# Performance work log

Measured on AMD Instinct MI355X. Metric: run time of the kernel, lower is better.

Reference implementation:

```python
import jax, jax.numpy as jnp
import numpy as np

N = 50000   # num_nodes
R = 16      # num_relations
B = 4       # num_bases = ceil(sqrt(R))
D = 128     # input_dim == output_dim -> vertical stacking path
E = 1_600_000  # num_edges = N * avg_degree(32)


def setup_inputs() -> dict:
    key = jax.random.key(0)
    ks = jax.random.split(key, 7)
    x = jax.random.normal(ks[0], (N, D), dtype=jnp.float32)
    source = jax.random.randint(ks[1], (E,), 0, N)
    target = jax.random.randint(ks[2], (E,), 0, N)
    edge_type = jax.random.randint(ks[3], (E,), 0, R)
    edge_weights = jax.random.uniform(ks[4], (E,), dtype=jnp.float32)
    # LowRankRepresentation params: weight (R, B) via uniform_norm_p1_ (uniform, L1-normalized),
    # bases (B, D, D) via xavier_normal_
    w = jax.random.uniform(ks[5], (R, B), dtype=jnp.float32)
    base_weights = w / jnp.sum(w, axis=-1, keepdims=True)
    xavier_std = (2.0 / (D + D)) ** 0.5
    bases = jax.random.normal(ks[6], (B, D, D), dtype=jnp.float32) * xavier_std
    return dict(x=x, source=source, target=target, edge_type=edge_type,
                edge_weights=edge_weights, base_weights=base_weights, bases=bases)


def reference(x, source, target, edge_type, edge_weights, base_weights, bases):
    # BasesDecomposition.forward, vertical stacking (input_dim == output_dim):
    #   adj: (R*N, N) sparse COO with indices (edge_type*N + target, source), values edge_weights
    #   h = spmm(adj, x)                -> (R*N, D), duplicate edges summed
    #   out = einsum('rb,bio,rni->no')  -> (N, D)
    num_nodes = x.shape[0]
    num_relations = base_weights.shape[0]
    seg = edge_type * num_nodes + target            # row index in stacked adjacency
    msgs = x[source] * edge_weights[:, None]        # (E, D) gathered + weighted messages
    h = jax.ops.segment_sum(msgs, seg, num_segments=num_relations * num_nodes)
    h = h.reshape(num_relations, num_nodes, -1)     # (R, N, D)
    return jnp.einsum('rb,bio,rni->no', base_weights, bases, h)
```

## Files before the change

### kernel.cpp

```cpp
#include <hip/hip_runtime.h>

#define NN 50000
#define NR 16
#define NB 4
#define DD 128
#define CAP 96

typedef __attribute__((ext_vector_type(8))) short bf16x8;
typedef __attribute__((ext_vector_type(4))) float f32x4;

static const size_t OFF_REC = (size_t)1 << 20;
static const size_t OFF_G   = (size_t)40 << 20;
static const size_t OFF_WF  = (size_t)96 << 20;

static __device__ __forceinline__ unsigned short f2bf(float f) {
    unsigned int u = __float_as_uint(f);
    unsigned int r = (u + 0x7FFF + ((u >> 16) & 1)) >> 16;
    return (unsigned short)r;
}

__global__ void fill_kernel(const int* __restrict__ src, const int* __restrict__ tgt,
                            const int* __restrict__ et, const float* __restrict__ ew,
                            int* __restrict__ cnt, int2* __restrict__ rec, int E) {
    int e = blockIdx.x * blockDim.x + threadIdx.x;
    if (e >= E) return;
    int t = tgt[e];
    int pos = atomicAdd(&cnt[t], 1);
    if (pos < CAP) {
        int2 r;
        r.x = src[e] | (et[e] << 16);
        r.y = __float_as_int(ew[e]);
        rec[t * CAP + pos] = r;
    }
}

__global__ void prep_kernel(const float* __restrict__ W, unsigned short* __restrict__ Wf) {
    int t = blockIdx.x * 256 + threadIdx.x;
    int lane = t & 63;
    int ft = t >> 6;
    int ks = ft >> 3, nt = ft & 7;
    int col = nt * 16 + (lane & 15);
    int k0 = ks * 32 + (lane >> 4) * 8;
    union { unsigned short v[8]; uint4 u; } pk;
#pragma unroll
    for (int j = 0; j < 8; ++j) pk.v[j] = f2bf(W[(size_t)(k0 + j) * DD + col]);
    ((uint4*)Wf)[t] = pk.u;
}

__global__ __launch_bounds__(256) void agg_kernel(const float* __restrict__ x,
                                                  const float* __restrict__ bw,
                                                  const int* __restrict__ cnt,
                                                  const int2* __restrict__ rec,
                                                  unsigned int* __restrict__ g) {
    __shared__ float sbw[NR * NB];
    int tid = threadIdx.x;
    if (tid < NR * NB) sbw[tid] = bw[tid];
    __syncthreads();

    int wave = tid >> 6;
    int lane = tid & 63;
    int n = blockIdx.x * 4 + wave;

    int deg = cnt[n];
    if (deg > CAP) deg = CAP;

    float2 acc[NB];
#pragma unroll
    for (int b = 0; b < NB; ++b) acc[b] = make_float2(0.f, 0.f);

    const int2* r = rec + (size_t)n * CAP;
    int j = 0;
    for (; j + 4 <= deg; j += 4) {
        int4 ra = *(const int4*)&r[j];
        int4 rb = *(const int4*)&r[j + 2];
        float2 xv0 = *(const float2*)&x[(size_t)(ra.x & 0xFFFF) * DD + lane * 2];
        float2 xv1 = *(const float2*)&x[(size_t)(ra.z & 0xFFFF) * DD + lane * 2];
        float2 xv2 = *(const float2*)&x[(size_t)(rb.x & 0xFFFF) * DD + lane * 2];
        float2 xv3 = *(const float2*)&x[(size_t)(rb.z & 0xFFFF) * DD + lane * 2];
        float w0 = __int_as_float(ra.y); int e0 = ra.x >> 16;
        float w1 = __int_as_float(ra.w); int e1 = ra.z >> 16;
        float w2 = __int_as_float(rb.y); int e2 = rb.x >> 16;
        float w3 = __int_as_float(rb.w); int e3 = rb.z >> 16;
#pragma unroll
        for (int b = 0; b < NB; ++b) {
            float c0 = w0 * sbw[e0 * NB + b];
            float c1 = w1 * sbw[e1 * NB + b];
            float c2 = w2 * sbw[e2 * NB + b];
            float c3 = w3 * sbw[e3 * NB + b];
            acc[b].x += c0 * xv0.x + c1 * xv1.x + c2 * xv2.x + c3 * xv3.x;
            acc[b].y += c0 * xv0.y + c1 * xv1.y + c2 * xv2.y + c3 * xv3.y;
        }
    }
    for (; j < deg; ++j) {
        int2 rc = r[j];
        int s = rc.x & 0xFFFF;
        int e = rc.x >> 16;
        float w = __int_as_float(rc.y);
        float2 xv = *(const float2*)&x[(size_t)s * DD + lane * 2];
#pragma unroll
        for (int b = 0; b < NB; ++b) {
            float c = w * sbw[e * NB + b];
            acc[b].x += c * xv.x;
            acc[b].y += c * xv.y;
        }
    }

    unsigned int* go = g + (size_t)n * (NB * DD / 2);
#pragma unroll
    for (int b = 0; b < NB; ++b) {
        unsigned int w = (unsigned int)f2bf(acc[b].x) | ((unsigned int)f2bf(acc[b].y) << 16);
        go[b * 64 + lane] = w;
    }
}

__global__ __launch_bounds__(256) void gemm_mfma(const unsigned short* __restrict__ g,
                                                 const unsigned short* __restrict__ Wf,
                                                 float* __restrict__ out) {
    int tid = threadIdx.x;
    int wid = tid >> 6;
    int lane = tid & 63;
    int rt = blockIdx.x * 4 + wid;
    if (rt >= (NN + 15) / 16) return;
    int row0 = rt * 16;

    const bf16x8* ga = (const bf16x8*)(g + (size_t)(row0 + (lane & 15)) * 512);
    const bf16x8* wb = (const bf16x8*)Wf;
    int kgrp = lane >> 4;

    f32x4 acc[8];
#pragma unroll
    for (int nt = 0; nt < 8; ++nt) acc[nt] = (f32x4){0.f, 0.f, 0.f, 0.f};

#pragma unroll
    for (int ks = 0; ks < 16; ++ks) {
        bf16x8 a = ga[ks * 4 + kgrp];
#pragma unroll
        for (int nt = 0; nt < 8; ++nt) {
            bf16x8 b = wb[(ks * 8 + nt) * 64 + lane];
            acc[nt] = __builtin_amdgcn_mfma_f32_16x16x32_bf16(a, b, acc[nt], 0, 0, 0);
        }
    }

    int col = lane & 15;
#pragma unroll
    for (int nt = 0; nt < 8; ++nt) {
#pragma unroll
        for (int q = 0; q < 4; ++q) {
            int row = row0 + kgrp * 4 + q;
            out[(size_t)row * DD + nt * 16 + col] = acc[nt][q];
        }
    }
}

extern "C" void kernel_launch(void* const* d_in, const int* in_sizes, int n_in,
                              void* d_out, int out_size, void* d_ws, size_t ws_size,
                              hipStream_t stream) {
    const float* x   = (const float*)d_in[0];
    const int* src   = (const int*)d_in[1];
    const int* tgt   = (const int*)d_in[2];
    const int* et    = (const int*)d_in[3];
    const float* ew  = (const float*)d_in[4];
    const float* bw  = (const float*)d_in[5];
    const float* bas = (const float*)d_in[6];
    float* out = (float*)d_out;

    int E = in_sizes[1];

    char* ws = (char*)d_ws;
    int*  cnt = (int*)ws;
    int2* rec = (int2*)(ws + OFF_REC);
    unsigned int*   gw = (unsigned int*)(ws + OFF_G);
    unsigned short* gs = (unsigned short*)(ws + OFF_G);
    unsigned short* Wf = (unsigned short*)(ws + OFF_WF);

    hipMemsetAsync(cnt, 0, NN * sizeof(int), stream);

    fill_kernel<<<(E + 255) / 256, 256, 0, stream>>>(src, tgt, et, ew, cnt, rec, E);
    prep_kernel<<<32, 256, 0, stream>>>(bas, Wf);

    agg_kernel<<<NN / 4, 256, 0, stream>>>(x, bw, cnt, rec, gw);

    gemm_mfma<<<(NN / 16 + 3) / 4, 256, 0, stream>>>(gs, Wf, out);
}
```

Before: 331.9 us.

## Build exact CSR via count/scan/scatter and gather bf16 copy of x

```diff
diff --git a/kernel.cpp b/kernel.cpp
--- a/kernel.cpp
+++ b/kernel.cpp
@@ -4,34 +4,112 @@
 #define NR 16
 #define NB 4
 #define DD 128
-#define CAP 96
+#define NBLK_S 196
 
 typedef __attribute__((ext_vector_type(8))) short bf16x8;
 typedef __attribute__((ext_vector_type(4))) float f32x4;
 
-static const size_t OFF_REC = (size_t)1 << 20;
+static const size_t OFF_EB  = (size_t)1 << 20;
+static const size_t OFF_CUR = (size_t)2 << 20;
+static const size_t OFF_BS  = (size_t)3 << 20;
+static const size_t OFF_REC = (size_t)4 << 20;
 static const size_t OFF_G   = (size_t)40 << 20;
 static const size_t OFF_WF  = (size_t)96 << 20;
+static const size_t OFF_XB  = (size_t)97 << 20;
 
 static __device__ __forceinline__ unsigned short f2bf(float f) {
     unsigned int u = __float_as_uint(f);
     unsigned int r = (u + 0x7FFF + ((u >> 16) & 1)) >> 16;
     return (unsigned short)r;
 }
-
-__global__ void fill_kernel(const int* __restrict__ src, const int* __restrict__ tgt,
-                            const int* __restrict__ et, const float* __restrict__ ew,
-                            int* __restrict__ cnt, int2* __restrict__ rec, int E) {
-    int e = blockIdx.x * blockDim.x + threadIdx.x;
-    if (e >= E) return;
-    int t = tgt[e];
-    int pos = atomicAdd(&cnt[t], 1);
-    if (pos < CAP) {
-        int2 r;
-        r.x = src[e] | (et[e] << 16);
-        r.y = __float_as_int(ew[e]);
-        rec[t * CAP + pos] = r;
-    }
+static __device__ __forceinline__ float blo(unsigned int u) { return __uint_as_float(u << 16); }
+static __device__ __forceinline__ float bhi(unsigned int u) { return __uint_as_float(u & 0xFFFF0000u); }
+
+__global__ void count_kernel(const int* __restrict__ tgt, int* __restrict__ cnt, int E) {
+    int e4 = blockIdx.x * 256 + threadIdx.x;
+    if (e4 * 4 < E) {
+        int4 t4 = ((const int4*)tgt)[e4];
+        atomicAdd(&cnt[t4.x], 1);
+        atomicAdd(&cnt[t4.y], 1);
+        atomicAdd(&cnt[t4.z], 1);
+        atomicAdd(&cnt[t4.w], 1);
+    }
+}
+
+__global__ __launch_bounds__(256) void scan1_kernel(const int* __restrict__ cnt,
+                                                    int* __restrict__ eloc,
+                                                    int* __restrict__ bsum) {
+    __shared__ int s[256];
+    int tid = threadIdx.x;
+    int n = blockIdx.x * 256 + tid;
+    int v = (n < NN) ? cnt[n] : 0;
+    s[tid] = v;
+    __syncthreads();
+#pragma unroll
+    for (int off = 1; off < 256; off <<= 1) {
+        int t = (tid >= off) ? s[tid - off] : 0;
+        __syncthreads();
+        s[tid] += t;
+        __syncthreads();
+    }
+    if (n < NN) eloc[n] = s[tid] - v;
+    if (tid == 255) bsum[blockIdx.x] = s[255];
+}
+
+__global__ __launch_bounds__(256) void scan2_kernel(const int* __restrict__ bsum,
+                                                    int* __restrict__ bbase) {
+    __shared__ int s[256];
+    int tid = threadIdx.x;
+    int v = (tid < NBLK_S) ? bsum[tid] : 0;
+    s[tid] = v;
+    __syncthreads();
+#pragma unroll
+    for (int off = 1; off < 256; off <<= 1) {
+        int t = (tid >= off) ? s[tid - off] : 0;
+        __syncthreads();
+        s[tid] += t;
+        __syncthreads();
+    }
+    if (tid < NBLK_S) bbase[tid] = s[tid] - v;
+}
+
+__global__ __launch_bounds__(256) void scan3_kernel(int* __restrict__ eloc,
+                                                    const int* __restrict__ bbase,
+                                                    int* __restrict__ cursor) {
+    int n = blockIdx.x * 256 + threadIdx.x;
+    if (n < NN) {
+        int e = eloc[n] + bbase[blockIdx.x];
+        eloc[n] = e;
+        cursor[n] = e;
+    }
+}
+
+__global__ void scatter_kernel(const int* __restrict__ src, const int* __restrict__ tgt,
+                               const int* __restrict__ et, const float* __restrict__ ew,
+                               int* __restrict__ cursor, int2* __restrict__ rec, int E) {
+    int e4 = blockIdx.x * 256 + threadIdx.x;
+    if (e4 * 4 >= E) return;
+    int4 t4 = ((const int4*)tgt)[e4];
+    int4 s4 = ((const int4*)src)[e4];
+    int4 q4 = ((const int4*)et)[e4];
+    float4 w4 = ((const float4*)ew)[e4];
+#define PUT(TT, SS, QQ, WW) { int pos = atomicAdd(&cursor[TT], 1); \
+    int2 rr; rr.x = (SS) | ((QQ) << 16); rr.y = __float_as_int(WW); rec[pos] = rr; }
+    PUT(t4.x, s4.x, q4.x, w4.x)
+    PUT(t4.y, s4.y, q4.y, w4.y)
+    PUT(t4.z, s4.z, q4.z, w4.z)
+    PUT(t4.w, s4.w, q4.w, w4.w)
+#undef PUT
+}
+
+__global__ void xconv_kernel(const float* __restrict__ x, uint4* __restrict__ xb) {
+    int t = blockIdx.x * 256 + threadIdx.x;
+    const float4* xf = (const float4*)x;
+    float4 a = xf[t * 2], b = xf[t * 2 + 1];
+    union { unsigned short v[8]; uint4 u; } pk;
+    pk.v[0] = f2bf(a.x); pk.v[1] = f2bf(a.y); pk.v[2] = f2bf(a.z); pk.v[3] = f2bf(a.w);
+    pk.v[4] = f2bf(b.x); pk.v[5] = f2bf(b.y); pk.v[6] = f2bf(b.z); pk.v[7] = f2bf(b.w);
+    xb[t] = pk.u;
 }
 
 __global__ void prep_kernel(const float* __restrict__ W, unsigned short* __restrict__ Wf) {
@@ -47,61 +125,60 @@
     ((uint4*)Wf)[t] = pk.u;
 }
 
-__global__ __launch_bounds__(256) void agg_kernel(const float* __restrict__ x,
-                                                  const float* __restrict__ bw,
-                                                  const int* __restrict__ cnt,
-                                                  const int2* __restrict__ rec,
-                                                  unsigned int* __restrict__ g) {
+__global__ __launch_bounds__(256) void agg3_kernel(const unsigned int* __restrict__ xb,
+                                                   const float* __restrict__ bw,
+                                                   const int* __restrict__ cnt,
+                                                   const int* __restrict__ ebase,
+                                                   const int2* __restrict__ rec,
+                                                   unsigned int* __restrict__ g) {
     __shared__ float sbw[NR * NB];
     int tid = threadIdx.x;
     if (tid < NR * NB) sbw[tid] = bw[tid];
     __syncthreads();
 
-    int wave = tid >> 6;
-    int lane = tid & 63;
-    int n = blockIdx.x * 4 + wave;
+    int wid = tid >> 6, lane = tid & 63;
+    int n = blockIdx.x * 4 + wid;
 
     int deg = cnt[n];
-    if (deg > CAP) deg = CAP;
+    const int2* rc = rec + ebase[n];
 
     float2 acc[NB];
 #pragma unroll
     for (int b = 0; b < NB; ++b) acc[b] = make_float2(0.f, 0.f);
 
-    const int2* r = rec + (size_t)n * CAP;
     int j = 0;
     for (; j + 4 <= deg; j += 4) {
-        int4 ra = *(const int4*)&r[j];
-        int4 rb = *(const int4*)&r[j + 2];
-        float2 xv0 = *(const float2*)&x[(size_t)(ra.x & 0xFFFF) * DD + lane * 2];
-        float2 xv1 = *(const float2*)&x[(size_t)(ra.z & 0xFFFF) * DD + lane * 2];
-        float2 xv2 = *(const float2*)&x[(size_t)(rb.x & 0xFFFF) * DD + lane * 2];
-        float2 xv3 = *(const float2*)&x[(size_t)(rb.z & 0xFFFF) * DD + lane * 2];
-        float w0 = __int_as_float(ra.y); int e0 = ra.x >> 16;
-        float w1 = __int_as_float(ra.w); int e1 = ra.z >> 16;
-        float w2 = __int_as_float(rb.y); int e2 = rb.x >> 16;
-        float w3 = __int_as_float(rb.w); int e3 = rb.z >> 16;
+        int2 r0 = rc[j], r1 = rc[j + 1], r2 = rc[j + 2], r3 = rc[j + 3];
+        unsigned int u0 = xb[(size_t)(r0.x & 0xFFFF) * 64 + lane];
+        unsigned int u1 = xb[(size_t)(r1.x & 0xFFFF) * 64 + lane];
+        unsigned int u2 = xb[(size_t)(r2.x & 0xFFFF) * 64 + lane];
+        unsigned int u3 = xb[(size_t)(r3.x & 0xFFFF) * 64 + lane];
+        float w0 = __int_as_float(r0.y); int e0 = (r0.x >> 16) & 15;
+        float w1 = __int_as_float(r1.y); int e1 = (r1.x >> 16) & 15;
+        float w2 = __int_as_float(r2.y); int e2 = (r2.x >> 16) & 15;
+        float w3 = __int_as_float(r3.y); int e3 = (r3.x >> 16) & 15;
+        float x0l = blo(u0), x0h = bhi(u0), x1l = blo(u1), x1h = bhi(u1);
+        float x2l = blo(u2), x2h = bhi(u2), x3l = blo(u3), x3h = bhi(u3);
 #pragma unroll
         for (int b = 0; b < NB; ++b) {
             float c0 = w0 * sbw[e0 * NB + b];
             float c1 = w1 * sbw[e1 * NB + b];
             float c2 = w2 * sbw[e2 * NB + b];
             float c3 = w3 * sbw[e3 * NB + b];
-            acc[b].x += c0 * xv0.x + c1 * xv1.x + c2 * xv2.x + c3 * xv3.x;
-            acc[b].y += c0 * xv0.y + c1 * xv1.y + c2 * xv2.y + c3 * xv3.y;
+            acc[b].x += c0 * x0l + c1 * x1l + c2 * x2l + c3 * x3l;
+            acc[b].y += c0 * x0h + c1 * x1h + c2 * x2h + c3 * x3h;
         }
     }
     for (; j < deg; ++j) {
-        int2 rc = r[j];
-        int s = rc.x & 0xFFFF;
-        int e = rc.x >> 16;
-        float w = __int_as_float(rc.y);
-        float2 xv = *(const float2*)&x[(size_t)s * DD + lane * 2];
+        int2 r = rc[j];
+        unsigned int u = xb[(size_t)(r.x & 0xFFFF) * 64 + lane];
+        float w = __int_as_float(r.y); int e = (r.x >> 16) & 15;
+        float xl = blo(u), xh = bhi(u);
 #pragma unroll
         for (int b = 0; b < NB; ++b) {
             float c = w * sbw[e * NB + b];
-            acc[b].x += c * xv.x;
-            acc[b].y += c * xv.y;
+            acc[b].x += c * xl;
+            acc[b].y += c * xh;
         }
     }
 
@@ -167,18 +244,29 @@
     int E = in_sizes[1];
 
     char* ws = (char*)d_ws;
-    int*  cnt = (int*)ws;
-    int2* rec = (int2*)(ws + OFF_REC);
-    unsigned int*   gw = (unsigned int*)(ws + OFF_G);
-    unsigned short* gs = (unsigned short*)(ws + OFF_G);
-    unsigned short* Wf = (unsigned short*)(ws + OFF_WF);
+    int*  cnt    = (int*)ws;
+    int*  ebase  = (int*)(ws + OFF_EB);
+    int*  cursor = (int*)(ws + OFF_CUR);
+    int*  bsum   = (int*)(ws + OFF_BS);
+    int*  bbase  = bsum + 256;
+    int2* rec    = (int2*)(ws + OFF_REC);
+    unsigned int*   gw  = (unsigned int*)(ws + OFF_G);
+    unsigned short* gs  = (unsigned short*)(ws + OFF_G);
+    unsigned short* Wf  = (unsigned short*)(ws + OFF_WF);
+    unsigned int*   xbw = (unsigned int*)(ws + OFF_XB);
 
     hipMemsetAsync(cnt, 0, NN * sizeof(int), stream);
 
-    fill_kernel<<<(E + 255) / 256, 256, 0, stream>>>(src, tgt, et, ew, cnt, rec, E);
+    count_kernel<<<(E / 4 + 255) / 256, 256, 0, stream>>>(tgt, cnt, E);
+    scan1_kernel<<<NBLK_S, 256, 0, stream>>>(cnt, ebase, bsum);
+    scan2_kernel<<<1, 256, 0, stream>>>(bsum, bbase);
+    scan3_kernel<<<NBLK_S, 256, 0, stream>>>(ebase, bbase, cursor);
+    scatter_kernel<<<(E / 4 + 255) / 256, 256, 0, stream>>>(src, tgt, et, ew, cursor, rec, E);
+
     prep_kernel<<<32, 256, 0, stream>>>(bas, Wf);
-
-    agg_kernel<<<NN / 4, 256, 0, stream>>>(x, bw, cnt, rec, gw);
+    xconv_kernel<<<3125, 256, 0, stream>>>(x, (uint4*)xbw);
+
+    agg3_kernel<<<NN / 4, 256, 0, stream>>>(xbw, bw, cnt, ebase, rec, gw);
 
     gemm_mfma<<<(NN / 16 + 3) / 4, 256, 0, stream>>>(gs, Wf, out);
 }
```

Result: slower. 379.0 us (+14.2%).

## Gather bf16 copy of node features and vectorize edge bucketing by four

Applied to the files above, without the earlier changes.

```diff
diff --git a/kernel.cpp b/kernel.cpp
--- a/kernel.cpp
+++ b/kernel.cpp
@@ -12,26 +12,43 @@
 static const size_t OFF_REC = (size_t)1 << 20;
 static const size_t OFF_G   = (size_t)40 << 20;
 static const size_t OFF_WF  = (size_t)96 << 20;
+static const size_t OFF_XB  = (size_t)97 << 20;
 
 static __device__ __forceinline__ unsigned short f2bf(float f) {
     unsigned int u = __float_as_uint(f);
     unsigned int r = (u + 0x7FFF + ((u >> 16) & 1)) >> 16;
     return (unsigned short)r;
 }
+static __device__ __forceinline__ float blo(unsigned int u) { return __uint_as_float(u << 16); }
+static __device__ __forceinline__ float bhi(unsigned int u) { return __uint_as_float(u & 0xFFFF0000u); }
 
 __global__ void fill_kernel(const int* __restrict__ src, const int* __restrict__ tgt,
                             const int* __restrict__ et, const float* __restrict__ ew,
                             int* __restrict__ cnt, int2* __restrict__ rec, int E) {
-    int e = blockIdx.x * blockDim.x + threadIdx.x;
-    if (e >= E) return;
-    int t = tgt[e];
-    int pos = atomicAdd(&cnt[t], 1);
-    if (pos < CAP) {
-        int2 r;
-        r.x = src[e] | (et[e] << 16);
-        r.y = __float_as_int(ew[e]);
-        rec[t * CAP + pos] = r;
-    }
+    int e4 = blockIdx.x * 256 + threadIdx.x;
+    if (e4 * 4 >= E) return;
+    int4 t4 = ((const int4*)tgt)[e4];
+    int4 s4 = ((const int4*)src)[e4];
+    int4 q4 = ((const int4*)et)[e4];
+    float4 w4 = ((const float4*)ew)[e4];
+#define PUT(TT, SS, QQ, WW) { int pos = atomicAdd(&cnt[TT], 1); \
+    if (pos < CAP) { int2 rr; rr.x = (SS) | ((QQ) << 16); rr.y = __float_as_int(WW); \
+    rec[(size_t)(TT) * CAP + pos] = rr; } }
+    PUT(t4.x, s4.x, q4.x, w4.x)
+    PUT(t4.y, s4.y, q4.y, w4.y)
+    PUT(t4.z, s4.z, q4.z, w4.z)
+    PUT(t4.w, s4.w, q4.w, w4.w)
+#undef PUT
+}
+
+__global__ void xconv_kernel(const float* __restrict__ x, uint4* __restrict__ xb) {
+    int t = blockIdx.x * 256 + threadIdx.x;
+    const float4* xf = (const float4*)x;
+    float4 a = xf[t * 2], b = xf[t * 2 + 1];
+    union { unsigned short v[8]; uint4 u; } pk;
+    pk.v[0] = f2bf(a.x); pk.v[1] = f2bf(a.y); pk.v[2] = f2bf(a.z); pk.v[3] = f2bf(a.w);
+    pk.v[4] = f2bf(b.x); pk.v[5] = f2bf(b.y); pk.v[6] = f2bf(b.z); pk.v[7] = f2bf(b.w);
+    xb[t] = pk.u;
 }
 
 __global__ void prep_kernel(const float* __restrict__ W, unsigned short* __restrict__ Wf) {
@@ -47,7 +64,7 @@
     ((uint4*)Wf)[t] = pk.u;
 }
 
-__global__ __launch_bounds__(256) void agg_kernel(const float* __restrict__ x,
+__global__ __launch_bounds__(256) void agg_kernel(const unsigned int* __restrict__ xb,
                                                   const float* __restrict__ bw,
                                                   const int* __restrict__ cnt,
                                                   const int2* __restrict__ rec,
@@ -57,51 +74,51 @@
     if (tid < NR * NB) sbw[tid] = bw[tid];
     __syncthreads();
 
-    int wave = tid >> 6;
-    int lane = tid & 63;
-    int n = blockIdx.x * 4 + wave;
+    int wid = tid >> 6, lane = tid & 63;
+    int n = blockIdx.x * 4 + wid;
 
     int deg = cnt[n];
     if (deg > CAP) deg = CAP;
+    const int2* rc = rec + (size_t)n * CAP;
 
     float2 acc[NB];
 #pragma unroll
     for (int b = 0; b < NB; ++b) acc[b] = make_float2(0.f, 0.f);
 
-    const int2* r = rec + (size_t)n * CAP;
     int j = 0;
     for (; j + 4 <= deg; j += 4) {
-        int4 ra = *(const int4*)&r[j];
-        int4 rb = *(const int4*)&r[j + 2];
-        float2 xv0 = *(const float2*)&x[(size_t)(ra.x & 0xFFFF) * DD + lane * 2];
-        float2 xv1 = *(const float2*)&x[(size_t)(ra.z & 0xFFFF) * DD + lane * 2];
-        float2 xv2 = *(const float2*)&x[(size_t)(rb.x & 0xFFFF) * DD + lane * 2];
-        float2 xv3 = *(const float2*)&x[(size_t)(rb.z & 0xFFFF) * DD + lane * 2];
-        float w0 = __int_as_float(ra.y); int e0 = ra.x >> 16;
-        float w1 = __int_as_float(ra.w); int e1 = ra.z >> 16;
-        float w2 = __int_as_float(rb.y); int e2 = rb.x >> 16;
-        float w3 = __int_as_float(rb.w); int e3 = rb.z >> 16;
+        int4 ra = *(const int4*)&rc[j];
+        int4 rb = *(const int4*)&rc[j + 2];
+        unsigned int u0 = xb[(size_t)(ra.x & 0xFFFF) * 64 + lane];
+        unsigned int u1 = xb[(size_t)(ra.z & 0xFFFF) * 64 + lane];
+        unsigned int u2 = xb[(size_t)(rb.x & 0xFFFF) * 64 + lane];
+        unsigned int u3 = xb[(size_t)(rb.z & 0xFFFF) * 64 + lane];
+        float w0 = __int_as_float(ra.y); int e0 = (ra.x >> 16) & 15;
+        float w1 = __int_as_float(ra.w); int e1 = (ra.z >> 16) & 15;
+        float w2 = __int_as_float(rb.y); int e2 = (rb.x >> 16) & 15;
+        float w3 = __int_as_float(rb.w); int e3 = (rb.z >> 16) & 15;
+        float x0l = blo(u0), x0h = bhi(u0), x1l = blo(u1), x1h = bhi(u1);
+        float x2l = blo(u2), x2h = bhi(u2), x3l = blo(u3), x3h = bhi(u3);
 #pragma unroll
         for (int b = 0; b < NB; ++b) {
             float c0 = w0 * sbw[e0 * NB + b];
             float c1 = w1 * sbw[e1 * NB + b];
             float c2 = w2 * sbw[e2 * NB + b];
             float c3 = w3 * sbw[e3 * NB + b];
-            acc[b].x += c0 * xv0.x + c1 * xv1.x + c2 * xv2.x + c3 * xv3.x;
-            acc[b].y += c0 * xv0.y + c1 * xv1.y + c2 * xv2.y + c3 * xv3.y;
+            acc[b].x += c0 * x0l + c1 * x1l + c2 * x2l + c3 * x3l;
+            acc[b].y += c0 * x0h + c1 * x1h + c2 * x2h + c3 * x3h;
         }
     }
     for (; j < deg; ++j) {
-        int2 rc = r[j];
-        int s = rc.x & 0xFFFF;
-        int e = rc.x >> 16;
-        float w = __int_as_float(rc.y);
-        float2 xv = *(const float2*)&x[(size_t)s * DD + lane * 2];
+        int2 r = rc[j];
+        unsigned int u = xb[(size_t)(r.x & 0xFFFF) * 64 + lane];
+        float w = __int_as_float(r.y); int e = (r.x >> 16) & 15;
+        float xl = blo(u), xh = bhi(u);
 #pragma unroll
         for (int b = 0; b < NB; ++b) {
             float c = w * sbw[e * NB + b];
-            acc[b].x += c * xv.x;
-            acc[b].y += c * xv.y;
+            acc[b].x += c * xl;
+            acc[b].y += c * xh;
         }
     }
 
@@ -169,16 +186,18 @@
     char* ws = (char*)d_ws;
     int*  cnt = (int*)ws;
     int2* rec = (int2*)(ws + OFF_REC);
-    unsigned int*   gw = (unsigned int*)(ws + OFF_G);
-    unsigned short* gs = (unsigned short*)(ws + OFF_G);
-    unsigned short* Wf = (unsigned short*)(ws + OFF_WF);
+    unsigned int*   gw  = (unsigned int*)(ws + OFF_G);
+    unsigned short* gs  = (unsigned short*)(ws + OFF_G);
+    unsigned short* Wf  = (unsigned short*)(ws + OFF_WF);
+    unsigned int*   xbw = (unsigned int*)(ws + OFF_XB);
 
     hipMemsetAsync(cnt, 0, NN * sizeof(int), stream);
 
-    fill_kernel<<<(E + 255) / 256, 256, 0, stream>>>(src, tgt, et, ew, cnt, rec, E);
+    fill_kernel<<<(E / 4 + 255) / 256, 256, 0, stream>>>(src, tgt, et, ew, cnt, rec, E);
     prep_kernel<<<32, 256, 0, stream>>>(bas, Wf);
-
-    agg_kernel<<<NN / 4, 256, 0, stream>>>(x, bw, cnt, rec, gw);
+    xconv_kernel<<<3125, 256, 0, stream>>>(x, (uint4*)xbw);
+
+    agg_kernel<<<NN / 4, 256, 0, stream>>>(xbw, bw, cnt, rec, gw);
 
     gemm_mfma<<<(NN / 16 + 3) / 4, 256, 0, stream>>>(gs, Wf, out);
 }
```

Result: faster. 315.4 us (-5.0%).
